# Kernel tuning notes

Hardware: AMD Instinct MI355X
Metric: run time of the kernel (lower is better)

## Reference

```python
import jax, jax.numpy as jnp
import numpy as np
from jax import lax

B, S, D_IN = 4, 4096, 1024
D_FAST, D_SLOW = 512, 512
Z_BIAS_FAST, Z_BIAS_SLOW = 2.0, -2.0


def _binop(q_i, q_j):
    a_i, b_i = q_i
    a_j, b_j = q_j
    return (a_i * a_j, a_j * b_i + b_j)


def parallel_scan(a, b):
    # h_t = a_t * h_{t-1} + b_t along seq axis (axis=1)
    _, h = lax.associative_scan(_binop, (a, b), axis=1)
    return h


def setup_inputs() -> dict:
    key = jax.random.key(0)
    ks = jax.random.split(key, 6)
    scale = 0.02
    x = jax.random.normal(ks[0], (B, S, D_IN), dtype=jnp.float32)
    W_zf = jax.random.normal(ks[1], (D_IN, D_FAST), dtype=jnp.float32) * scale
    b_zf = jnp.full((D_FAST,), Z_BIAS_FAST, dtype=jnp.float32)
    W_hf = jax.random.normal(ks[2], (D_IN, D_FAST), dtype=jnp.float32) * scale
    b_hf = jnp.zeros((D_FAST,), dtype=jnp.float32)
    W_zs = jax.random.normal(ks[3], (D_IN, D_SLOW), dtype=jnp.float32) * scale
    b_zs = jnp.full((D_SLOW,), Z_BIAS_SLOW, dtype=jnp.float32)
    W_hs = jax.random.normal(ks[4], (D_IN, D_SLOW), dtype=jnp.float32) * scale
    b_hs = jnp.zeros((D_SLOW,), dtype=jnp.float32)
    W_g = jax.random.normal(ks[5], (D_FAST + D_SLOW, D_FAST + D_SLOW), dtype=jnp.float32) * scale
    b_g = jnp.zeros((D_FAST + D_SLOW,), dtype=jnp.float32)
    return {"x": x, "W_zf": W_zf, "b_zf": b_zf, "W_hf": W_hf, "b_hf": b_hf,
            "W_zs": W_zs, "b_zs": b_zs, "W_hs": W_hs, "b_hs": b_hs,
            "W_g": W_g, "b_g": b_g}


def reference(x, W_zf, b_zf, W_hf, b_hf, W_zs, b_zs, W_hs, b_hs, W_g, b_g):
    # Fast compartment (coupling='output' => slow branch sees raw x)
    z_fast = jax.nn.sigmoid(jnp.einsum('bsd,df->bsf', x, W_zf) + b_zf)
    h_tilde_fast = jnp.einsum('bsd,df->bsf', x, W_hf) + b_hf
    h_fast = parallel_scan(1.0 - z_fast, z_fast * h_tilde_fast)

    # Slow compartment
    z_slow = jax.nn.sigmoid(jnp.einsum('bsd,df->bsf', x, W_zs) + b_zs)
    h_tilde_slow = jnp.einsum('bsd,df->bsf', x, W_hs) + b_hs
    h_slow = parallel_scan(1.0 - z_slow, z_slow * h_tilde_slow)

    h_combined = jnp.concatenate([h_fast, h_slow], axis=-1)  # (B, S, D_FAST+D_SLOW)
    gate = jax.nn.sigmoid(jnp.einsum('bsc,cd->bsd', h_combined, W_g) + b_g)
    return gate * h_combined
```

## Files before the change

kernel.cpp:

```cpp
#include <hip/hip_runtime.h>

#define BB 4
#define SS 4096
#define DIN 1024
#define DH 1024
#define PN 2048
#define MM (BB*SS)
#define NC 64
#define CL 64

typedef unsigned short ushort_t;
typedef __attribute__((ext_vector_type(8))) short bf16x8;
typedef __attribute__((ext_vector_type(4))) float f32x4;
typedef __attribute__((ext_vector_type(4))) unsigned short u16x4;

__device__ inline float bf2f(ushort_t u) {
    union { float f; unsigned int i; } v; v.i = ((unsigned int)u) << 16; return v.f;
}
__device__ inline ushort_t f2bf(float f) {
    union { float f; unsigned int i; } v; v.f = f;
    unsigned int r = v.i + 0x7fffu + ((v.i >> 16) & 1u);
    return (ushort_t)(r >> 16);
}
__device__ inline float sigmoidf_(float x) { return 1.0f / (1.0f + __expf(-x)); }

__device__ inline void load_lds16(const void* g, void* l) {
    __builtin_amdgcn_global_load_lds(
        (const __attribute__((address_space(1))) void*)g,
        (__attribute__((address_space(3))) void*)l, 16, 0, 0);
}

__global__ void zero_out_kernel(float* out, int n) {
    int i = blockIdx.x * 256 + threadIdx.x;
    if (i < n) out[i] = 0.0f;
}

#define PREP_NBLK 17160
__global__ __launch_bounds__(256) void prep_kernel(
    const float* __restrict__ x,
    const float* __restrict__ Wzf, const float* __restrict__ Wzs,
    const float* __restrict__ Whf, const float* __restrict__ Whs,
    const float* __restrict__ Wg,
    const float* __restrict__ bzf, const float* __restrict__ bzs,
    const float* __restrict__ bhf, const float* __restrict__ bhs,
    ushort_t* __restrict__ WcatT, ushort_t* __restrict__ WgT,
    ushort_t* __restrict__ Xb, float* __restrict__ bcat)
{
    __shared__ ushort_t tile[64][65];
    const int bx = blockIdx.x, tid = threadIdx.x;

    if (bx < 768) {
        const float* src; ushort_t* dst; int srcN, t;
        if (bx < 512) {
            int wi = bx >> 7; t = bx & 127; srcN = 512;
            const float* S[4] = {Wzf, Wzs, Whf, Whs};
            src = S[wi];
            dst = WcatT + (size_t)(wi * 512) * DIN;
        } else {
            t = bx - 512; srcN = 1024; src = Wg; dst = WgT;
        }
        const int k0 = (t & 15) * 64, n0 = (t >> 4) * 64;
        const int tx = tid & 63, ty = tid >> 6;
        #pragma unroll
        for (int i = ty; i < 64; i += 4)
            tile[i][tx] = f2bf(src[(size_t)(k0 + i) * srcN + n0 + tx]);
        __syncthreads();
        #pragma unroll
        for (int i = ty; i < 64; i += 4)
            dst[(size_t)(n0 + i) * DIN + k0 + tx] = tile[tx][i];
    } else if (bx < 17152) {
        size_t i = ((size_t)(bx - 768) * 256 + tid) * 4;
        float4 v = *(const float4*)(x + i);
        u16x4 o;
        o.x = f2bf(v.x); o.y = f2bf(v.y); o.z = f2bf(v.z); o.w = f2bf(v.w);
        *(u16x4*)(Xb + i) = o;
    } else {
        int i = (bx - 17152) * 256 + tid;
        float v = (i < 512) ? bzf[i] : (i < 1024) ? bzs[i - 512]
                : (i < 1536) ? bhf[i - 1024] : bhs[i - 1536];
        bcat[i] = v;
    }
}

template <int EPI, int NB>
__global__ __launch_bounds__(256) void gemm_kernel(
    const ushort_t* __restrict__ A, const ushort_t* __restrict__ Bt,
    int K, int lda,
    const float* __restrict__ bias,
    ushort_t* __restrict__ Zarr, ushort_t* __restrict__ Harr,
    const float* __restrict__ bg, const ushort_t* __restrict__ Hbf,
    float* __restrict__ Out)
{
    __shared__ alignas(16) ushort_t As[128 * 64];
    __shared__ alignas(16) ushort_t Bs[128 * 64];

    const int tid  = threadIdx.x;
    const int lane = tid & 63;
    const int wave = tid >> 6;
    const int wm   = wave & 1;
    const int wn   = wave >> 1;
    const int lrow = lane & 15;
    const int kgrp = lane >> 4;

    const int id  = blockIdx.x;
    const int xcd = id & 7;
    const int s   = id >> 3;
    const int mBase = (xcd + 8 * (s / NB)) * 128;
    const int nBase = (s % NB) * 128;

    f32x4 acc[4][4] = {};

    const ushort_t* Ablk = A  + (size_t)mBase * lda;
    const ushort_t* Bblk = Bt + (size_t)nBase * K;

    for (int k0 = 0; k0 < K; k0 += 64) {
        #pragma unroll
        for (int i = 0; i < 4; i++) {
            int idx = i * 256 + tid;
            int r   = idx >> 3;
            int cc  = ((idx & 7) ^ (r & 7)) * 8;
            load_lds16(Ablk + (size_t)r * lda + k0 + cc, &As[idx * 8]);
            load_lds16(Bblk + (size_t)r * K   + k0 + cc, &Bs[idx * 8]);
        }
        __syncthreads();

        #pragma unroll
        for (int kk = 0; kk < 64; kk += 32) {
            const int c0 = (kk >> 3) + kgrp;
            bf16x8 af[4], bfr[4];
            #pragma unroll
            for (int mt = 0; mt < 4; mt++) {
                int r = wm * 64 + mt * 16 + lrow;
                af[mt] = *(const bf16x8*)&As[r * 64 + (c0 ^ (r & 7)) * 8];
            }
            #pragma unroll
            for (int nt = 0; nt < 4; nt++) {
                int r = wn * 64 + nt * 16 + lrow;
                bfr[nt] = *(const bf16x8*)&Bs[r * 64 + (c0 ^ (r & 7)) * 8];
            }
            #pragma unroll
            for (int mt = 0; mt < 4; mt++)
                #pragma unroll
                for (int nt = 0; nt < 4; nt++)
                    acc[mt][nt] = __builtin_amdgcn_mfma_f32_16x16x32_bf16(
                        af[mt], bfr[nt], acc[mt][nt], 0, 0, 0);
        }
        __syncthreads();
    }

    const int row0  = mBase + wm * 64;
    const int col0  = nBase + wn * 64;
    const int rquad = (lane >> 4) * 4;

    if (EPI == 0) {
        const bool isz = (nBase < DH);
        ushort_t* Dst  = isz ? Zarr : Harr;
        const int csub = isz ? 0 : DH;
        #pragma unroll
        for (int nt = 0; nt < 4; nt++) {
            int col  = col0 + nt * 16 + lrow;
            float bv = bias[col];
            int dcol = col - csub;
            #pragma unroll
            for (int mt = 0; mt < 4; mt++) {
                int row = row0 + mt * 16 + rquad;
                ushort_t* p = Dst + (size_t)row * DH + dcol;
                #pragma unroll
                for (int r = 0; r < 4; r++) {
                    float v = acc[mt][nt][r] + bv;
                    if (isz) v = sigmoidf_(v);
                    p[(size_t)r * DH] = f2bf(v);
                }
            }
        }
    } else {
        #pragma unroll
        for (int nt = 0; nt < 4; nt++) {
            int col  = col0 + nt * 16 + lrow;
            float bv = bg[col];
            #pragma unroll
            for (int mt = 0; mt < 4; mt++) {
                int row = row0 + mt * 16 + rquad;
                #pragma unroll
                for (int r = 0; r < 4; r++) {
                    float g = sigmoidf_(acc[mt][nt][r] + bv);
                    float h = bf2f(Hbf[(size_t)(row + r) * DH + col]);
                    Out[(size_t)(row + r) * DH + col] = g * h;
                }
            }
        }
    }
}

__global__ __launch_bounds__(256) void scan_chunk_agg(
    const ushort_t* __restrict__ Zarr, const ushort_t* __restrict__ Harr,
    float* __restrict__ Agg, float* __restrict__ Bagg)
{
    const int c4    = threadIdx.x * 4;
    const int chunk = blockIdx.x;
    const int b     = blockIdx.y;
    const size_t s0 = ((size_t)b * SS + (size_t)chunk * CL) * DH + c4;
    const ushort_t* Zp = Zarr + s0;
    const ushort_t* Hp = Harr + s0;

    float A0 = 1.0f, A1 = 1.0f, A2 = 1.0f, A3 = 1.0f;
    float B0 = 0.0f, B1 = 0.0f, B2 = 0.0f, B3 = 0.0f;
    #pragma unroll 8
    for (int t = 0; t < CL; t++) {
        u16x4 zv = *(const u16x4*)(Zp + (size_t)t * DH);
        u16x4 hv = *(const u16x4*)(Hp + (size_t)t * DH);
        float z0 = bf2f(zv.x), z1 = bf2f(zv.y), z2 = bf2f(zv.z), z3 = bf2f(zv.w);
        float h0 = bf2f(hv.x), h1 = bf2f(hv.y), h2 = bf2f(hv.z), h3 = bf2f(hv.w);
        A0 *= 1.0f - z0;  B0 = (1.0f - z0) * B0 + z0 * h0;
        A1 *= 1.0f - z1;  B1 = (1.0f - z1) * B1 + z1 * h1;
        A2 *= 1.0f - z2;  B2 = (1.0f - z2) * B2 + z2 * h2;
        A3 *= 1.0f - z3;  B3 = (1.0f - z3) * B3 + z3 * h3;
    }
    const size_t idx = ((size_t)(b * NC + chunk)) * DH + c4;
    *(float4*)(Agg  + idx) = make_float4(A0, A1, A2, A3);
    *(float4*)(Bagg + idx) = make_float4(B0, B1, B2, B3);
}

__global__ void scan_carry(const float* __restrict__ Agg, const float* __restrict__ Bagg,
                           float* __restrict__ Hinit)
{
    const int i = blockIdx.x * 256 + threadIdx.x;
    const int b = i >> 10, c = i & 1023;
    float h = 0.0f;
    for (int j = 0; j < NC; j++) {
        const size_t idx = ((size_t)(b * NC + j)) * DH + c;
        Hinit[idx] = h;
        h = Agg[idx] * h + Bagg[idx];
    }
}

__global__ __launch_bounds__(256) void scan_apply(
    const ushort_t* __restrict__ Zarr, ushort_t* Harr, const float* __restrict__ Hinit)
{
    const int c4    = threadIdx.x * 4;
    const int chunk = blockIdx.x;
    const int b     = blockIdx.y;
    const size_t s0 = ((size_t)b * SS + (size_t)chunk * CL) * DH + c4;
    const ushort_t* Zp = Zarr + s0;
    ushort_t*       Hp = Harr + s0;

    float4 hi = *(const float4*)(Hinit + ((size_t)(b * NC + chunk)) * DH + c4);
    float h0 = hi.x, h1 = hi.y, h2 = hi.z, h3 = hi.w;
    #pragma unroll 8
    for (int t = 0; t < CL; t++) {
        u16x4 zv = *(const u16x4*)(Zp + (size_t)t * DH);
        u16x4 hv = *(const u16x4*)(Hp + (size_t)t * DH);
        float z0 = bf2f(zv.x), z1 = bf2f(zv.y), z2 = bf2f(zv.z), z3 = bf2f(zv.w);
        float t0 = bf2f(hv.x), t1 = bf2f(hv.y), t2 = bf2f(hv.z), t3 = bf2f(hv.w);
        h0 = (1.0f - z0) * h0 + z0 * t0;
        h1 = (1.0f - z1) * h1 + z1 * t1;
        h2 = (1.0f - z2) * h2 + z2 * t2;
        h3 = (1.0f - z3) * h3 + z3 * t3;
        u16x4 o;
        o.x = f2bf(h0); o.y = f2bf(h1); o.z = f2bf(h2); o.w = f2bf(h3);
        *(u16x4*)(Hp + (size_t)t * DH) = o;
    }
}

extern "C" void kernel_launch(void* const* d_in, const int* in_sizes, int n_in,
                              void* d_out, int out_size, void* d_ws, size_t ws_size,
                              hipStream_t stream)
{
    const float* x   = (const float*)d_in[0];
    const float* Wzf = (const float*)d_in[1];
    const float* bzf = (const float*)d_in[2];
    const float* Whf = (const float*)d_in[3];
    const float* bhf = (const float*)d_in[4];
    const float* Wzs = (const float*)d_in[5];
    const float* bzs = (const float*)d_in[6];
    const float* Whs = (const float*)d_in[7];
    const float* bhs = (const float*)d_in[8];
    const float* Wg  = (const float*)d_in[9];
    const float* bg  = (const float*)d_in[10];

    const size_t NEED = (size_t)42 << 20;
    if (ws_size < NEED) {
        zero_out_kernel<<<(MM * DH + 255) / 256, 256, 0, stream>>>((float*)d_out, MM * DH);
        return;
    }

    char* ws = (char*)d_ws;
    ushort_t* WcatT = (ushort_t*)(ws);
    ushort_t* WgT   = (ushort_t*)(ws + ((size_t)4 << 20));
    float*    bcat  = (float*)   (ws + ((size_t)6 << 20));
    float*    Agg   = (float*)   (ws + ((size_t)6 << 20) + (64 << 10));
    float*    Bagg  = (float*)   (ws + ((size_t)7 << 20) + (64 << 10));
    float*    Hinit = (float*)   (ws + ((size_t)8 << 20) + (64 << 10));
    ushort_t* Harr  = (ushort_t*)(ws + ((size_t)10 << 20));

    ushort_t* Xb   = (ushort_t*)d_out;
    ushort_t* Zarr = Xb + (size_t)MM * DH;

    dim3 blk(256);

    prep_kernel<<<PREP_NBLK, blk, 0, stream>>>(
        x, Wzf, Wzs, Whf, Whs, Wg, bzf, bzs, bhf, bhs, WcatT, WgT, Xb, bcat);

    gemm_kernel<0, PN / 128><<<(MM / 128) * (PN / 128), blk, 0, stream>>>(
        Xb, WcatT, DIN, DIN, bcat, Zarr, Harr, nullptr, nullptr, nullptr);

    scan_chunk_agg<<<dim3(NC, BB), blk, 0, stream>>>(Zarr, Harr, Agg, Bagg);
    scan_carry<<<16, 256, 0, stream>>>(Agg, Bagg, Hinit);
    scan_apply<<<dim3(NC, BB), blk, 0, stream>>>(Zarr, Harr, Hinit);

    gemm_kernel<1, DH / 128><<<(MM / 128) * (DH / 128), blk, 0, stream>>>(
        Harr, WgT, DIN, DH, nullptr, nullptr, nullptr, bg, Harr,
        (float*)d_out);
}
```

Measured before the change: 329.6 us.

## Rewrite GEMM as 256x256 tile, 8-wave, double-buffered ping-pong pipeline

Both GEMMs move from 128x128 tiles with 4 waves and a single LDS buffer to 256x256 tiles with 8 waves and double-buffered LDS. Global-to-LDS loads are split into eight phases, each overlapped with the MFMAs on one quadrant, using raw s_barrier, vmcnt waits and setprio. The aim is to raise arithmetic intensity and hide load latency behind compute. In exchange, LDS use grows to 128KB per block and more registers are needed, and the ktn wraparound issues redundant loads on the last iteration.

After: 338.2 us. 2.6% more time.

```diff
diff --git a/kernel.cpp b/kernel.cpp
--- a/kernel.cpp
+++ b/kernel.cpp
@@ -82,8 +82,59 @@
     }
 }
 
+#define VM4 asm volatile("s_waitcnt vmcnt(4)" ::: "memory")
+
+#define STG_A(b, h, kt) { \
+    _Pragma("unroll") \
+    for (int j = 0; j < 2; j++) { \
+        int c = wave * 2 + j; \
+        load_lds16(Ablk + (size_t)((h) * 128 + c * 8) * lda + (kt) * 64 + laneAOff, \
+                   &As[(b) * 16384 + (h) * 8192 + c * 512]); \
+    } }
+
+#define STG_B(b, h, kt) { \
+    _Pragma("unroll") \
+    for (int j = 0; j < 2; j++) { \
+        int c = wave * 2 + j; \
+        load_lds16(Bblk + (size_t)((h) * 128 + c * 8) * K + (kt) * 64 + laneBOff, \
+                   &Bs[(b) * 16384 + (h) * 8192 + c * 512]); \
+    } }
+
+#define PHASE(b, qm, qn, STAGE, TAIL) { \
+    bf16x8 af[4][2], bq[2][2]; \
+    _Pragma("unroll") \
+    for (int mt = 0; mt < 4; mt++) { \
+        _Pragma("unroll") \
+        for (int kh = 0; kh < 2; kh++) { \
+            int r = (qm) * 128 + wm * 64 + mt * 16 + lrow; \
+            af[mt][kh] = *(const bf16x8*)&As[(b) * 16384 + r * 64 + (((kh * 4 + kgrp) ^ (lrow & 7)) * 8)]; \
+        } } \
+    _Pragma("unroll") \
+    for (int nt = 0; nt < 2; nt++) { \
+        _Pragma("unroll") \
+        for (int kh = 0; kh < 2; kh++) { \
+            int r = (qn) * 128 + wn * 32 + nt * 16 + lrow; \
+            bq[nt][kh] = *(const bf16x8*)&Bs[(b) * 16384 + r * 64 + (((kh * 4 + kgrp) ^ (lrow & 7)) * 8)]; \
+        } } \
+    STAGE; \
+    asm volatile("s_barrier" ::: "memory"); \
+    __builtin_amdgcn_s_setprio(1); \
+    _Pragma("unroll") \
+    for (int mt = 0; mt < 4; mt++) { \
+        _Pragma("unroll") \
+        for (int nt = 0; nt < 2; nt++) { \
+            acc[qm][qn][mt][nt] = __builtin_amdgcn_mfma_f32_16x16x32_bf16( \
+                af[mt][0], bq[nt][0], acc[qm][qn][mt][nt], 0, 0, 0); \
+            acc[qm][qn][mt][nt] = __builtin_amdgcn_mfma_f32_16x16x32_bf16( \
+                af[mt][1], bq[nt][1], acc[qm][qn][mt][nt], 0, 0, 0); \
+        } } \
+    __builtin_amdgcn_s_setprio(0); \
+    TAIL; \
+    asm volatile("s_barrier" ::: "memory"); \
+  }
+
 template <int EPI, int NB>
-__global__ __launch_bounds__(256) void gemm_kernel(
+__global__ __launch_bounds__(512, 2) void gemm_kernel(
     const ushort_t* __restrict__ A, const ushort_t* __restrict__ Bt,
     int K, int lda,
     const float* __restrict__ bias,
@@ -91,8 +142,8 @@
     const float* __restrict__ bg, const ushort_t* __restrict__ Hbf,
     float* __restrict__ Out)
 {
-    __shared__ alignas(16) ushort_t As[128 * 64];
-    __shared__ alignas(16) ushort_t Bs[128 * 64];
+    __shared__ alignas(16) ushort_t As[2 * 256 * 64];
+    __shared__ alignas(16) ushort_t Bs[2 * 256 * 64];
 
     const int tid  = threadIdx.x;
     const int lane = tid & 63;
@@ -105,51 +156,38 @@
     const int id  = blockIdx.x;
     const int xcd = id & 7;
     const int s   = id >> 3;
-    const int mBase = (xcd + 8 * (s / NB)) * 128;
-    const int nBase = (s % NB) * 128;
-
-    f32x4 acc[4][4] = {};
+    const int mBase = (xcd + 8 * (s / NB)) * 256;
+    const int nBase = (s % NB) * 256;
+
+    f32x4 acc[2][2][4][2] = {};
 
     const ushort_t* Ablk = A  + (size_t)mBase * lda;
     const ushort_t* Bblk = Bt + (size_t)nBase * K;
-
-    for (int k0 = 0; k0 < K; k0 += 64) {
-        #pragma unroll
-        for (int i = 0; i < 4; i++) {
-            int idx = i * 256 + tid;
-            int r   = idx >> 3;
-            int cc  = ((idx & 7) ^ (r & 7)) * 8;
-            load_lds16(Ablk + (size_t)r * lda + k0 + cc, &As[idx * 8]);
-            load_lds16(Bblk + (size_t)r * K   + k0 + cc, &Bs[idx * 8]);
-        }
-        __syncthreads();
-
-        #pragma unroll
-        for (int kk = 0; kk < 64; kk += 32) {
-            const int c0 = (kk >> 3) + kgrp;
-            bf16x8 af[4], bfr[4];
-            #pragma unroll
-            for (int mt = 0; mt < 4; mt++) {
-                int r = wm * 64 + mt * 16 + lrow;
-                af[mt] = *(const bf16x8*)&As[r * 64 + (c0 ^ (r & 7)) * 8];
-            }
-            #pragma unroll
-            for (int nt = 0; nt < 4; nt++) {
-                int r = wn * 64 + nt * 16 + lrow;
-                bfr[nt] = *(const bf16x8*)&Bs[r * 64 + (c0 ^ (r & 7)) * 8];
-            }
-            #pragma unroll
-            for (int mt = 0; mt < 4; mt++)
-                #pragma unroll
-                for (int nt = 0; nt < 4; nt++)
-                    acc[mt][nt] = __builtin_amdgcn_mfma_f32_16x16x32_bf16(
-                        af[mt], bfr[nt], acc[mt][nt], 0, 0, 0);
-        }
-        __syncthreads();
-    }
-
-    const int row0  = mBase + wm * 64;
-    const int col0  = nBase + wn * 64;
+    const int laneAOff = (lane >> 3) * lda + (((lane & 7) ^ (lane >> 3)) * 8);
+    const int laneBOff = (lane >> 3) * K   + (((lane & 7) ^ (lane >> 3)) * 8);
+
+    const int NKT = K >> 6;
+    const int NIT = NKT >> 1;
+
+    STG_A(0, 0, 0); STG_B(0, 0, 0); STG_A(0, 1, 0); STG_B(0, 1, 0);
+    STG_A(1, 0, 1); STG_B(1, 0, 1);
+    VM4;
+    asm volatile("s_barrier" ::: "memory");
+
+    for (int i = 0; i < NIT; i++) {
+        const int kt1  = 2 * i + 1;
+        const int ktn0 = (2 * i + 2) & (NKT - 1);
+        const int ktn1 = (2 * i + 3) & (NKT - 1);
+        PHASE(0, 0, 0, STG_A(1, 1, kt1),  );
+        PHASE(0, 0, 1, STG_B(1, 1, kt1),  );
+        PHASE(0, 1, 0, STG_A(0, 0, ktn0), );
+        PHASE(0, 1, 1, STG_B(0, 0, ktn0), VM4);
+        PHASE(1, 0, 0, STG_A(0, 1, ktn0), );
+        PHASE(1, 0, 1, STG_B(0, 1, ktn0), );
+        PHASE(1, 1, 0, STG_A(1, 0, ktn1), );
+        PHASE(1, 1, 1, STG_B(1, 0, ktn1), VM4);
+    }
+
     const int rquad = (lane >> 4) * 4;
 
     if (EPI == 0) {
@@ -157,17 +195,21 @@
         ushort_t* Dst  = isz ? Zarr : Harr;
         const int csub = isz ? 0 : DH;
         #pragma unroll
-        for (int nt = 0; nt < 4; nt++) {
-            int col  = col0 + nt * 16 + lrow;
+        for (int qm = 0; qm < 2; qm++)
+        #pragma unroll
+        for (int qn = 0; qn < 2; qn++)
+        #pragma unroll
+        for (int nt = 0; nt < 2; nt++) {
+            int col  = nBase + qn * 128 + wn * 32 + nt * 16 + lrow;
             float bv = bias[col];
             int dcol = col - csub;
             #pragma unroll
             for (int mt = 0; mt < 4; mt++) {
-                int row = row0 + mt * 16 + rquad;
+                int row = mBase + qm * 128 + wm * 64 + mt * 16 + rquad;
                 ushort_t* p = Dst + (size_t)row * DH + dcol;
                 #pragma unroll
                 for (int r = 0; r < 4; r++) {
-                    float v = acc[mt][nt][r] + bv;
+                    float v = acc[qm][qn][mt][nt][r] + bv;
                     if (isz) v = sigmoidf_(v);
                     p[(size_t)r * DH] = f2bf(v);
                 }
@@ -175,15 +217,19 @@
         }
     } else {
         #pragma unroll
-        for (int nt = 0; nt < 4; nt++) {
-            int col  = col0 + nt * 16 + lrow;
+        for (int qm = 0; qm < 2; qm++)
+        #pragma unroll
+        for (int qn = 0; qn < 2; qn++)
+        #pragma unroll
+        for (int nt = 0; nt < 2; nt++) {
+            int col  = nBase + qn * 128 + wn * 32 + nt * 16 + lrow;
             float bv = bg[col];
             #pragma unroll
             for (int mt = 0; mt < 4; mt++) {
-                int row = row0 + mt * 16 + rquad;
+                int row = mBase + qm * 128 + wm * 64 + mt * 16 + rquad;
                 #pragma unroll
                 for (int r = 0; r < 4; r++) {
-                    float g = sigmoidf_(acc[mt][nt][r] + bv);
+                    float g = sigmoidf_(acc[qm][qn][mt][nt][r] + bv);
                     float h = bf2f(Hbf[(size_t)(row + r) * DH + col]);
                     Out[(size_t)(row + r) * DH + col] = g * h;
                 }
@@ -301,14 +347,14 @@
     prep_kernel<<<PREP_NBLK, blk, 0, stream>>>(
         x, Wzf, Wzs, Whf, Whs, Wg, bzf, bzs, bhf, bhs, WcatT, WgT, Xb, bcat);
 
-    gemm_kernel<0, PN / 128><<<(MM / 128) * (PN / 128), blk, 0, stream>>>(
+    gemm_kernel<0, PN / 256><<<(MM / 256) * (PN / 256), dim3(512), 0, stream>>>(
         Xb, WcatT, DIN, DIN, bcat, Zarr, Harr, nullptr, nullptr, nullptr);
 
     scan_chunk_agg<<<dim3(NC, BB), blk, 0, stream>>>(Zarr, Harr, Agg, Bagg);
     scan_carry<<<16, 256, 0, stream>>>(Agg, Bagg, Hinit);
     scan_apply<<<dim3(NC, BB), blk, 0, stream>>>(Zarr, Harr, Hinit);
 
-    gemm_kernel<1, DH / 128><<<(MM / 128) * (DH / 128), blk, 0, stream>>>(
+    gemm_kernel<1, DH / 256><<<(MM / 256) * (DH / 256), dim3(512), 0, stream>>>(
         Harr, WgT, DIN, DH, nullptr, nullptr, nullptr, bg, Harr,
         (float*)d_out);
 }
```
